# Kernel tuning notes

Measured on AMD Instinct MI355X. Metric: run time of the kernel, lower is better.

## Reference

```python
import jax, jax.numpy as jnp
import numpy as np

INPUT, OUTPUT, HIDDEN, EMBED = 20000, 2048, 1024, 512
BATCH, NUM_GENES = 512, 20000

def _linear_init(key, fan_in, fan_out):
    kw, kb = jax.random.split(key)
    bound = 1.0 / np.sqrt(fan_in)
    W = jax.random.uniform(kw, (fan_out, fan_in), minval=-bound, maxval=bound, dtype=jnp.float32)
    b = jax.random.uniform(kb, (fan_out,), minval=-bound, maxval=bound, dtype=jnp.float32)
    return W, b

def setup_inputs() -> dict:
    key = jax.random.key(0)
    kx, ke, k1, k2, k3 = jax.random.split(key, 5)
    x = jax.random.normal(kx, (BATCH, INPUT), dtype=jnp.float32)
    embedding_x = jax.random.normal(ke, (NUM_GENES, EMBED), dtype=jnp.float32)
    W_ge, b_ge = _linear_init(k1, INPUT, HIDDEN)   # gene_expander Linear
    W_em, b_em = _linear_init(k2, EMBED, HIDDEN)   # embed_mlp Linear
    W_c, b_c = _linear_init(k3, 2 * HIDDEN, OUTPUT)  # combiner Linear
    return {"x": x, "embedding_x": embedding_x, "W_ge": W_ge, "b_ge": b_ge,
            "W_em": W_em, "b_em": b_em, "W_c": W_c, "b_c": b_c}

def reference(x, embedding_x, W_ge, b_ge, W_em, b_em, W_c, b_c):
    lrelu = lambda v: jax.nn.leaky_relu(v, negative_slope=0.01)
    # gene_expander: [B, input] -> [B, hidden]
    x_expanded = lrelu(x @ W_ge.T + b_ge)
    # embed_mlp (dropout = identity at eval): [G, embed] -> [G, hidden]
    gene_embeddings = lrelu(embedding_x @ W_em.T + b_em)
    # softmax over features, then batched GEMM replaces the per-sample loop
    num_genes = min(x.shape[1], gene_embeddings.shape[0])
    weights = jax.nn.softmax(x, axis=1)
    weighted_embeddings = weights[:, :num_genes] @ gene_embeddings[:num_genes]  # [B, hidden]
    combined = jnp.concatenate([x_expanded, weighted_embeddings], axis=1)  # [B, 2*hidden]
    return lrelu(combined @ W_c.T + b_c)  # [B, output]
```

## Files before the change

kernel.cpp:

```cpp
#include <hip/hip_runtime.h>
#include <hip/hip_bf16.h>
#include <stdint.h>

#define BATCH  512
#define INPUT  20000
#define KPAD   20032
#define NPADE  20096
#define HIDDEN 1024
#define EMBED  512
#define NOUT   2048

typedef __attribute__((ext_vector_type(8))) __bf16 bf16x8;
typedef __attribute__((ext_vector_type(8))) unsigned short u16x8;
typedef __attribute__((ext_vector_type(4))) unsigned short u16x4;
typedef __attribute__((ext_vector_type(4))) float f32x4;

static __device__ __forceinline__ unsigned short f2bf(float f) {
  uint32_t u = __builtin_bit_cast(uint32_t, f);
  u += 0x7fffu + ((u >> 16) & 1u);
  return (unsigned short)(u >> 16);
}

static __device__ __forceinline__ void g2l16(const unsigned short* g, unsigned short* l) {
  __builtin_amdgcn_global_load_lds(
      (const __attribute__((address_space(1))) void*)g,
      (__attribute__((address_space(3))) void*)l, 16, 0, 0);
}

__global__ __launch_bounds__(256) void convert_kernel(
    const float* __restrict__ src, unsigned short* __restrict__ dst,
    int rows, int cols, int rowsPad, int colsPad)
{
  const int cpc = colsPad >> 3;
  const int nchunks = rowsPad * cpc;
  for (int idx = blockIdx.x * 256 + threadIdx.x; idx < nchunks; idx += gridDim.x * 256) {
    int row = idx / cpc;
    int c0  = (idx - row * cpc) << 3;
    u16x8 v = {};
    if (row < rows && c0 < cols) {
      const float* p = src + (size_t)row * cols + c0;
      f32x4 f0 = *reinterpret_cast<const f32x4*>(p);
      f32x4 f1 = *reinterpret_cast<const f32x4*>(p + 4);
      v[0] = f2bf(f0[0]); v[1] = f2bf(f0[1]); v[2] = f2bf(f0[2]); v[3] = f2bf(f0[3]);
      v[4] = f2bf(f1[0]); v[5] = f2bf(f1[1]); v[6] = f2bf(f1[2]); v[7] = f2bf(f1[3]);
    }
    *reinterpret_cast<u16x8*>(dst + (size_t)row * colsPad + c0) = v;
  }
}

template<int EPI, int FUSED, int ZBITS>
__global__ __launch_bounds__(256) void gemm97(
    const unsigned short* __restrict__ A0, const unsigned short* __restrict__ B0,
    const unsigned short* __restrict__ A1, const unsigned short* __restrict__ B1,
    int lda, int ldb,
    const float* __restrict__ bias,
    void* __restrict__ Cp, int ldc, int pstride,
    int M, int N, int Nw, int K, int kChunk)
{
  __shared__ __align__(16) unsigned short As[128 * 64];
  __shared__ __align__(16) unsigned short Bs[128 * 64];

  const int zall  = blockIdx.z;
  const int which = FUSED ? (zall >> ZBITS) : 0;
  const int z     = FUSED ? (zall & ((1 << ZBITS) - 1)) : zall;
  const unsigned short* A = (FUSED && which) ? A1 : A0;
  const unsigned short* B = (FUSED && which) ? B1 : B0;

  const int m0 = blockIdx.y * 128, n0 = blockIdx.x * 128;
  const int k0   = z * kChunk;
  const int kend = min(K, k0 + kChunk);
  const int tid = threadIdx.x;
  const int l = tid & 63, w = tid >> 6;

  const int srow = w * 32 + (l >> 3);
  const int scol = (l & 7) * 8;
  const unsigned short* ag = A + (size_t)(m0 + srow) * lda + scol;
  const unsigned short* bg = B + (size_t)(n0 + srow) * ldb + scol;

  const int wm = (w >> 1) * 64, wn = (w & 1) * 64;
  const int lr = l & 15, lk = (l >> 4) * 8;

  f32x4 acc[4][4] = {};

  for (int kb = k0; kb < kend; kb += 64) {
#pragma unroll
    for (int j = 0; j < 4; ++j)
      g2l16(ag + (size_t)j * 8 * lda + kb, As + (w * 32 + j * 8) * 64);
#pragma unroll
    for (int j = 0; j < 4; ++j)
      g2l16(bg + (size_t)j * 8 * ldb + kb, Bs + (w * 32 + j * 8) * 64);
    __syncthreads();
#pragma unroll
    for (int ks = 0; ks < 2; ++ks) {
      bf16x8 a[4], b[4];
#pragma unroll
      for (int i = 0; i < 4; ++i)
        a[i] = *reinterpret_cast<const bf16x8*>(&As[(wm + i * 16 + lr) * 64 + ks * 32 + lk]);
#pragma unroll
      for (int i = 0; i < 4; ++i)
        b[i] = *reinterpret_cast<const bf16x8*>(&Bs[(wn + i * 16 + lr) * 64 + ks * 32 + lk]);
#pragma unroll
      for (int mi = 0; mi < 4; ++mi)
#pragma unroll
        for (int ni = 0; ni < 4; ++ni)
          acc[mi][ni] = __builtin_amdgcn_mfma_f32_16x16x32_bf16(a[mi], b[ni], acc[mi][ni], 0, 0, 0);
    }
    __syncthreads();
  }

  const int rb = (l >> 4) * 4;
#pragma unroll
  for (int mi = 0; mi < 4; ++mi) {
#pragma unroll
    for (int ni = 0; ni < 4; ++ni) {
#pragma unroll
      for (int j = 0; j < 4; ++j) {
        int m = m0 + wm + mi * 16 + rb + j;
        int n = n0 + wn + ni * 16 + lr;
        float v = acc[mi][ni][j];
        if (EPI == 0) {
          if (n < Nw) {
            float t = v + bias[m];
            t = t > 0.f ? t : 0.01f * t;
            reinterpret_cast<unsigned short*>(Cp)[(size_t)m * ldc + n] =
                (n < N) ? f2bf(t) : (unsigned short)0;
          }
        } else {
          reinterpret_cast<float*>(Cp)[(size_t)z * pstride + (size_t)m * ldc +
                                       (FUSED ? which * 1024 : 0) + n] = v;
        }
      }
    }
  }
}

__global__ __launch_bounds__(256) void prep_x_kernel(
    const float* __restrict__ x,
    unsigned short* __restrict__ xb,
    unsigned short* __restrict__ wb)
{
  const int r = blockIdx.x;
  const int t = threadIdx.x;
  const float* xr = x + (size_t)r * INPUT;

  float m = -3.4e38f, s = 0.f;
  for (int c = t; c < INPUT / 4; c += 256) {
    float4 v = reinterpret_cast<const float4*>(xr)[c];
    float cm = fmaxf(fmaxf(v.x, v.y), fmaxf(v.z, v.w));
    if (cm > m) { s *= __expf(m - cm); m = cm; }
    s += __expf(v.x - m) + __expf(v.y - m) + __expf(v.z - m) + __expf(v.w - m);
  }
#pragma unroll
  for (int off = 32; off > 0; off >>= 1) {
    float om = __shfl_xor(m, off);
    float os = __shfl_xor(s, off);
    float nm = fmaxf(m, om);
    s = s * __expf(m - nm) + os * __expf(om - nm);
    m = nm;
  }
  __shared__ float sm[4], ss[4];
  if ((t & 63) == 0) { sm[t >> 6] = m; ss[t >> 6] = s; }
  __syncthreads();
  float M4 = fmaxf(fmaxf(sm[0], sm[1]), fmaxf(sm[2], sm[3]));
  float S4 = ss[0] * __expf(sm[0] - M4) + ss[1] * __expf(sm[1] - M4)
           + ss[2] * __expf(sm[2] - M4) + ss[3] * __expf(sm[3] - M4);
  float inv = 1.f / S4;

  unsigned short* xbr = xb + (size_t)r * KPAD;
  unsigned short* wbr = wb + (size_t)r * KPAD;
  for (int c = t; c < KPAD / 4; c += 256) {
    u16x4 xo = {}, wo = {};
    if (c < INPUT / 4) {
      float4 v = reinterpret_cast<const float4*>(xr)[c];
      xo[0] = f2bf(v.x); xo[1] = f2bf(v.y); xo[2] = f2bf(v.z); xo[3] = f2bf(v.w);
      wo[0] = f2bf(__expf(v.x - M4) * inv);
      wo[1] = f2bf(__expf(v.y - M4) * inv);
      wo[2] = f2bf(__expf(v.z - M4) * inv);
      wo[3] = f2bf(__expf(v.w - M4) * inv);
    }
    reinterpret_cast<u16x4*>(xbr)[c] = xo;
    reinterpret_cast<u16x4*>(wbr)[c] = wo;
  }
}

template<int S, int MODE>
__global__ __launch_bounds__(256) void reduce_kernel(
    const float* __restrict__ P, const float* __restrict__ bias, void* __restrict__ outp)
{
  size_t base = ((size_t)blockIdx.x * 256 + threadIdx.x) * 4;
  f32x4 s = {};
#pragma unroll
  for (int zz = 0; zz < S; ++zz)
    s += *reinterpret_cast<const f32x4*>(P + (size_t)zz * BATCH * NOUT + base);
  int n = (int)(base & (NOUT - 1));
  if (MODE == 0) {
    u16x4 o;
    if (n < 1024) {
#pragma unroll
      for (int j = 0; j < 4; ++j) {
        float v = s[j] + bias[n + j];
        v = v > 0.f ? v : 0.01f * v;
        o[j] = f2bf(v);
      }
    } else {
#pragma unroll
      for (int j = 0; j < 4; ++j) o[j] = f2bf(s[j]);
    }
    *reinterpret_cast<u16x4*>(reinterpret_cast<unsigned short*>(outp) + base) = o;
  } else {
    f32x4 o;
#pragma unroll
    for (int j = 0; j < 4; ++j) {
      float v = s[j] + bias[n + j];
      o[j] = v > 0.f ? v : 0.01f * v;
    }
    *reinterpret_cast<f32x4*>(reinterpret_cast<float*>(outp) + base) = o;
  }
}

extern "C" void kernel_launch(void* const* d_in, const int* in_sizes, int n_in,
                              void* d_out, int out_size, void* d_ws, size_t ws_size,
                              hipStream_t stream)
{
  const float* x    = (const float*)d_in[0];
  const float* emb  = (const float*)d_in[1];
  const float* W_ge = (const float*)d_in[2];
  const float* b_ge = (const float*)d_in[3];
  const float* W_em = (const float*)d_in[4];
  const float* b_em = (const float*)d_in[5];
  const float* W_c  = (const float*)d_in[6];
  const float* b_c  = (const float*)d_in[7];
  float* out = (float*)d_out;

  char* ws = (char*)d_ws;
  unsigned short* xb   = (unsigned short*)(ws);
  unsigned short* wb   = (unsigned short*)(ws + 20512768);
  unsigned short* Wgeb = (unsigned short*)(ws + 41025536);
  unsigned short* Et   = (unsigned short*)(ws + 82051072);
  unsigned short* Wcb  = (unsigned short*)(ws + 123076608);
  unsigned short* comb = (unsigned short*)(ws + 131465216);
  float*          P    = (float*)(ws + 133562368);
  unsigned short* embb = (unsigned short*)(ws + 133562368);
  unsigned short* Wemb = (unsigned short*)(ws + 133562368 + 20578304);

  convert_kernel<<<1024, 256, 0, stream>>>(emb,  embb, INPUT, EMBED, NPADE, EMBED);
  convert_kernel<<<256,  256, 0, stream>>>(W_em, Wemb, HIDDEN, EMBED, HIDDEN, EMBED);
  convert_kernel<<<1024, 256, 0, stream>>>(W_ge, Wgeb, HIDDEN, INPUT, HIDDEN, KPAD);
  convert_kernel<<<512,  256, 0, stream>>>(W_c,  Wcb,  NOUT, NOUT, NOUT, NOUT);

  prep_x_kernel<<<BATCH, 256, 0, stream>>>(x, xb, wb);

  gemm97<0, 0, 0><<<dim3(157, 8, 1), 256, 0, stream>>>(
      Wemb, embb, nullptr, nullptr, EMBED, EMBED, b_em,
      Et, KPAD, 0, HIDDEN, INPUT, KPAD, EMBED, EMBED);

  gemm97<1, 1, 4><<<dim3(8, 4, 32), 256, 0, stream>>>(
      xb, Wgeb, wb, Et, KPAD, KPAD, nullptr,
      P, NOUT, BATCH * NOUT, BATCH, 1024, 1024, KPAD, 1280);

  reduce_kernel<16, 0><<<(BATCH * NOUT / 4) / 256, 256, 0, stream>>>(P, b_ge, comb);

  gemm97<1, 0, 0><<<dim3(16, 4, 4), 256, 0, stream>>>(
      comb, Wcb, nullptr, nullptr, NOUT, NOUT, nullptr,
      P, NOUT, BATCH * NOUT, BATCH, NOUT, NOUT, NOUT, 512);

  reduce_kernel<4, 1><<<(BATCH * NOUT / 4) / 256, 256, 0, stream>>>(P, b_c, out);
}
```

Measured before the change: 256.4 us.

## Add double-buffered 256x256-tile MFMA GEMM for embed and fused K-split GEMMs

Introduces a new GEMM kernel with 256x256 output tiles, 512 threads (8 waves, each computing a 128x64 sub-tile), and double-buffered LDS staging via global_load_lds, so the next K-slice prefetch overlaps MFMA work. It replaces the 128x128 kernel for the embedding MLP GEMM and the fused gene-expander/weighted-embedding split-K GEMM, cutting redundant global/L2 reads of A and B panels. NPADE is raised so the gene dimension pads to a multiple of 256, and the workspace offset is shifted to match. The trade-off is 128 KB of LDS per block and large accumulator register use, which allows only one block per CU and a coarser grid with fewer blocks to hide latency.

```diff
diff --git a/kernel.cpp b/kernel.cpp
--- a/kernel.cpp
+++ b/kernel.cpp
@@ -5,7 +5,7 @@
 #define BATCH  512
 #define INPUT  20000
 #define KPAD   20032
-#define NPADE  20096
+#define NPADE  20224
 #define HIDDEN 1024
 #define EMBED  512
 #define NOUT   2048
@@ -45,6 +45,109 @@
       v[4] = f2bf(f1[0]); v[5] = f2bf(f1[1]); v[6] = f2bf(f1[2]); v[7] = f2bf(f1[3]);
     }
     *reinterpret_cast<u16x8*>(dst + (size_t)row * colsPad + c0) = v;
+  }
+}
+
+template<int EPI, int FUSED, int ZBITS>
+__global__ __launch_bounds__(512, 2) void gemm256(
+    const unsigned short* __restrict__ A0, const unsigned short* __restrict__ B0,
+    const unsigned short* __restrict__ A1, const unsigned short* __restrict__ B1,
+    int lda, int ldb,
+    const float* __restrict__ bias,
+    void* __restrict__ Cp, int ldc, int pstride,
+    int M, int N, int Nw, int K, int kChunk)
+{
+  __shared__ __align__(16) unsigned short As[2][256 * 64];
+  __shared__ __align__(16) unsigned short Bs[2][256 * 64];
+
+  const int zall  = blockIdx.z;
+  const int which = FUSED ? (zall >> ZBITS) : 0;
+  const int z     = FUSED ? (zall & ((1 << ZBITS) - 1)) : zall;
+  const unsigned short* A = (FUSED && which) ? A1 : A0;
+  const unsigned short* B = (FUSED && which) ? B1 : B0;
+
+  const int m0 = blockIdx.y * 256, n0 = blockIdx.x * 256;
+  const int k0   = z * kChunk;
+  const int kend = min(K, k0 + kChunk);
+  const int nt   = (kend - k0) >> 6;
+
+  const int tid = threadIdx.x;
+  const int l = tid & 63, w = tid >> 6;
+
+  const int srow = tid >> 3;
+  const int scol = (tid & 7) * 8;
+  const unsigned short* ag = A + (size_t)(m0 + srow) * lda + scol;
+  const unsigned short* bg = B + (size_t)(n0 + srow) * ldb + scol;
+
+  const int wr = w >> 2, wc = w & 3;
+  const int lr = l & 15, lk = (l >> 4) * 8;
+
+  f32x4 acc[8][4] = {};
+
+#define STAGE(buf, kb)                                                        \
+  do {                                                                        \
+    _Pragma("unroll")                                                         \
+    for (int r = 0; r < 4; ++r)                                               \
+      g2l16(ag + (size_t)(r * 64) * lda + (kb), &As[buf][(r * 64 + w * 8) * 64]); \
+    _Pragma("unroll")                                                         \
+    for (int r = 0; r < 4; ++r)                                               \
+      g2l16(bg + (size_t)(r * 64) * ldb + (kb), &Bs[buf][(r * 64 + w * 8) * 64]); \
+  } while (0)
+
+  STAGE(0, k0);
+  __syncthreads();
+
+  int cur = 0;
+  for (int t = 0; t < nt; ++t) {
+    if (t + 1 < nt) {
+      if (cur) STAGE(0, k0 + (t + 1) * 64);
+      else     STAGE(1, k0 + (t + 1) * 64);
+    }
+#pragma unroll
+    for (int ks = 0; ks < 2; ++ks) {
+      bf16x8 a[8], b[4];
+#pragma unroll
+      for (int i = 0; i < 8; ++i)
+        a[i] = *reinterpret_cast<const bf16x8*>(
+            &As[cur][(wr * 128 + i * 16 + lr) * 64 + ks * 32 + lk]);
+#pragma unroll
+      for (int i = 0; i < 4; ++i)
+        b[i] = *reinterpret_cast<const bf16x8*>(
+            &Bs[cur][(wc * 64 + i * 16 + lr) * 64 + ks * 32 + lk]);
+#pragma unroll
+      for (int mi = 0; mi < 8; ++mi)
+#pragma unroll
+        for (int ni = 0; ni < 4; ++ni)
+          acc[mi][ni] = __builtin_amdgcn_mfma_f32_16x16x32_bf16(a[mi], b[ni], acc[mi][ni], 0, 0, 0);
+    }
+    __syncthreads();
+    cur ^= 1;
+  }
+#undef STAGE
+
+  const int rb = (l >> 4) * 4;
+#pragma unroll
+  for (int mi = 0; mi < 8; ++mi) {
+#pragma unroll
+    for (int ni = 0; ni < 4; ++ni) {
+#pragma unroll
+      for (int j = 0; j < 4; ++j) {
+        int m = m0 + wr * 128 + mi * 16 + rb + j;
+        int n = n0 + wc * 64 + ni * 16 + lr;
+        float v = acc[mi][ni][j];
+        if (EPI == 0) {
+          if (n < Nw) {
+            float t2 = v + bias[m];
+            t2 = t2 > 0.f ? t2 : 0.01f * t2;
+            reinterpret_cast<unsigned short*>(Cp)[(size_t)m * ldc + n] =
+                (n < N) ? f2bf(t2) : (unsigned short)0;
+          }
+        } else {
+          reinterpret_cast<float*>(Cp)[(size_t)z * pstride + (size_t)m * ldc +
+                                       (FUSED ? which * 1024 : 0) + n] = v;
+        }
+      }
+    }
   }
 }
 
@@ -241,7 +344,7 @@
   unsigned short* comb = (unsigned short*)(ws + 131465216);
   float*          P    = (float*)(ws + 133562368);
   unsigned short* embb = (unsigned short*)(ws + 133562368);
-  unsigned short* Wemb = (unsigned short*)(ws + 133562368 + 20578304);
+  unsigned short* Wemb = (unsigned short*)(ws + 133562368 + 20709376);
 
   convert_kernel<<<1024, 256, 0, stream>>>(emb,  embb, INPUT, EMBED, NPADE, EMBED);
   convert_kernel<<<256,  256, 0, stream>>>(W_em, Wemb, HIDDEN, EMBED, HIDDEN, EMBED);
@@ -250,11 +353,11 @@
 
   prep_x_kernel<<<BATCH, 256, 0, stream>>>(x, xb, wb);
 
-  gemm97<0, 0, 0><<<dim3(157, 8, 1), 256, 0, stream>>>(
+  gemm256<0, 0, 0><<<dim3(79, 4, 1), 512, 0, stream>>>(
       Wemb, embb, nullptr, nullptr, EMBED, EMBED, b_em,
       Et, KPAD, 0, HIDDEN, INPUT, KPAD, EMBED, EMBED);
 
-  gemm97<1, 1, 4><<<dim3(8, 4, 32), 256, 0, stream>>>(
+  gemm256<1, 1, 4><<<dim3(4, 2, 32), 512, 0, stream>>>(
       xb, Wgeb, wb, Et, KPAD, KPAD, nullptr,
       P, NOUT, BATCH * NOUT, BATCH, 1024, 1024, KPAD, 1280);
 
```

Result: faster. 248.2 us (-3.2%).

## Replace big split-K GEMM with 256x256 double-buffered, 8-wave pipelined kernel

Applied to the files above, without the earlier changes.

The main fused split-K GEMM (x·W_ge and softmax·embeddings) moves from a 128x128, 4-wave, single-buffered kernel to a 256x256 tile with 8 waves and double-buffered LDS. Global-to-LDS loads for later K tiles are interleaved with four MFMA phases, using explicit waitcnt, barriers and s_setprio. The goal is to hide load latency and raise MFMA reuse per byte loaded. The cost is 128KB of LDS per block and far fewer blocks (256 vs 1024), which risks lower occupancy and load imbalance across CUs.

```diff
diff --git a/kernel.cpp b/kernel.cpp
--- a/kernel.cpp
+++ b/kernel.cpp
@@ -25,6 +25,238 @@
   __builtin_amdgcn_global_load_lds(
       (const __attribute__((address_space(1))) void*)g,
       (__attribute__((address_space(3))) void*)l, 16, 0, 0);
+}
+
+#define MFMA(a, b, c) __builtin_amdgcn_mfma_f32_16x16x32_bf16((a), (b), (c), 0, 0, 0)
+
+__global__ __launch_bounds__(512, 2) void gemm8p_fused(
+    const unsigned short* __restrict__ xb, const unsigned short* __restrict__ Wgeb,
+    const unsigned short* __restrict__ wb, const unsigned short* __restrict__ Etp,
+    float* __restrict__ P, int kChunk)
+{
+  __shared__ __align__(16) unsigned short As[2][2][128 * 64];
+  __shared__ __align__(16) unsigned short Bs[2][2][128 * 64];
+  unsigned short* AsW = &As[0][0][0];
+  unsigned short* BsW = &Bs[0][0][0];
+
+  const int which = blockIdx.z >> 4;
+  const int z     = blockIdx.z & 15;
+  const unsigned short* Ap = which ? wb  : xb;
+  const unsigned short* Bp = which ? Etp : Wgeb;
+
+  const int m0 = blockIdx.y * 256, n0 = blockIdx.x * 256;
+  const int k0   = z * kChunk;
+  const int kend = min(KPAD, k0 + kChunk);
+  const int nt   = (kend - k0) >> 6;
+
+  const int tid = threadIdx.x;
+  const int l = tid & 63, w = tid >> 6;
+  const int srow = tid >> 3, scol = (tid & 7) * 8;
+
+  const unsigned short* ag = Ap + (size_t)(m0 + srow) * KPAD + k0 + scol;
+  const unsigned short* bg = Bp + (size_t)(n0 + srow) * KPAD + k0 + scol;
+
+  const int wr = w >> 2, wc = w & 3;
+  const int lr = l & 15, lk = (l >> 4) * 8;
+
+  auto stA = [&](int buf, int h, int dk) {
+    const unsigned short* g = ag + (size_t)(h * 128) * KPAD + dk;
+    unsigned short* d = AsW + (buf * 2 + h) * 8192 + (w * 8) * 64;
+    g2l16(g, d);
+    g2l16(g + (size_t)64 * KPAD, d + 64 * 64);
+  };
+  auto stB = [&](int buf, int h, int dk) {
+    const unsigned short* g = bg + (size_t)(h * 128) * KPAD + dk;
+    unsigned short* d = BsW + (buf * 2 + h) * 8192 + (w * 8) * 64;
+    g2l16(g, d);
+    g2l16(g + (size_t)64 * KPAD, d + 64 * 64);
+  };
+  auto rdA = [&](int buf, int mi, int ks) -> bf16x8 {
+    return *reinterpret_cast<const bf16x8*>(
+        AsW + (buf * 2 + wr) * 8192 + (mi * 16 + lr) * 64 + ks * 32 + lk);
+  };
+  auto rdB = [&](int buf, int ni, int ks) -> bf16x8 {
+    return *reinterpret_cast<const bf16x8*>(
+        BsW + (buf * 2 + (wc >> 1)) * 8192 + ((wc & 1) * 64 + ni * 16 + lr) * 64 + ks * 32 + lk);
+  };
+
+  f32x4 acc[8][4] = {};
+
+  stA(0, 0, 0); stB(0, 0, 0); stA(0, 1, 0); stB(0, 1, 0);
+  if (nt > 1) {
+    stA(1, 0, 64); stB(1, 0, 64);
+    asm volatile("s_waitcnt vmcnt(4)" ::: "memory");
+  } else {
+    asm volatile("s_waitcnt vmcnt(0)" ::: "memory");
+  }
+  __builtin_amdgcn_s_barrier();
+
+  for (int t = 0; t < nt; ++t) {
+    const int buf = t & 1, nb = buf ^ 1;
+    const int dk1 = (t + 1) << 6, dk2 = (t + 2) << 6;
+    bf16x8 a0[4][2], a1[4][2], b0[2][2], b1[2][2];
+
+#pragma unroll
+    for (int mi = 0; mi < 4; ++mi) { a0[mi][0] = rdA(buf, mi, 0); a0[mi][1] = rdA(buf, mi, 1); }
+#pragma unroll
+    for (int ni = 0; ni < 2; ++ni) { b0[ni][0] = rdB(buf, ni, 0); b0[ni][1] = rdB(buf, ni, 1); }
+    if (t + 1 < nt) stA(nb, 1, dk1);
+    __builtin_amdgcn_s_barrier();
+    asm volatile("s_waitcnt lgkmcnt(0)" ::: "memory");
+    __builtin_amdgcn_sched_barrier(0);
+    __builtin_amdgcn_s_setprio(1);
+#pragma unroll
+    for (int mi = 0; mi < 4; ++mi)
+#pragma unroll
+      for (int ni = 0; ni < 2; ++ni) {
+        acc[mi][ni] = MFMA(a0[mi][0], b0[ni][0], acc[mi][ni]);
+        acc[mi][ni] = MFMA(a0[mi][1], b0[ni][1], acc[mi][ni]);
+      }
+    __builtin_amdgcn_s_setprio(0);
+    __builtin_amdgcn_s_barrier();
+
+#pragma unroll
+    for (int mi = 0; mi < 4; ++mi) { a1[mi][0] = rdA(buf, mi + 4, 0); a1[mi][1] = rdA(buf, mi + 4, 1); }
+    if (t + 1 < nt) stB(nb, 1, dk1);
+    __builtin_amdgcn_s_barrier();
+    asm volatile("s_waitcnt lgkmcnt(0)" ::: "memory");
+    __builtin_amdgcn_sched_barrier(0);
+    __builtin_amdgcn_s_setprio(1);
+#pragma unroll
+    for (int mi = 0; mi < 4; ++mi)
+#pragma unroll
+      for (int ni = 0; ni < 2; ++ni) {
+        acc[mi + 4][ni] = MFMA(a1[mi][0], b0[ni][0], acc[mi + 4][ni]);
+        acc[mi + 4][ni] = MFMA(a1[mi][1], b0[ni][1], acc[mi + 4][ni]);
+      }
+    __builtin_amdgcn_s_setprio(0);
+    __builtin_amdgcn_s_barrier();
+
+#pragma unroll
+    for (int ni = 0; ni < 2; ++ni) { b1[ni][0] = rdB(buf, ni + 2, 0); b1[ni][1] = rdB(buf, ni + 2, 1); }
+    if (t + 2 < nt) stA(buf, 0, dk2);
+    __builtin_amdgcn_s_barrier();
+    asm volatile("s_waitcnt lgkmcnt(0)" ::: "memory");
+    __builtin_amdgcn_sched_barrier(0);
+    __builtin_amdgcn_s_setprio(1);
+#pragma unroll
+    for (int mi = 0; mi < 4; ++mi)
+#pragma unroll
+      for (int ni = 0; ni < 2; ++ni) {
+        acc[mi + 4][ni + 2] = MFMA(a1[mi][0], b1[ni][0], acc[mi + 4][ni + 2]);
+        acc[mi + 4][ni + 2] = MFMA(a1[mi][1], b1[ni][1], acc[mi + 4][ni + 2]);
+      }
+    __builtin_amdgcn_s_setprio(0);
+    __builtin_amdgcn_s_barrier();
+
+    if (t + 2 < nt) stB(buf, 0, dk2);
+    __builtin_amdgcn_s_barrier();
+    __builtin_amdgcn_sched_barrier(0);
+    __builtin_amdgcn_s_setprio(1);
+#pragma unroll
+    for (int mi = 0; mi < 4; ++mi)
+#pragma unroll
+      for (int ni = 0; ni < 2; ++ni) {
+        acc[mi][ni + 2] = MFMA(a0[mi][0], b1[ni][0], acc[mi][ni + 2]);
+        acc[mi][ni + 2] = MFMA(a0[mi][1], b1[ni][1], acc[mi][ni + 2]);
+      }
+    __builtin_amdgcn_s_setprio(0);
+    if (t + 2 < nt)      asm volatile("s_waitcnt vmcnt(4)" ::: "memory");
+    else if (t + 1 < nt) asm volatile("s_waitcnt vmcnt(0)" ::: "memory");
+    __builtin_amdgcn_s_barrier();
+  }
+
+  const int rb = (l >> 4) * 4;
+  float* dst = P + (size_t)z * (BATCH * NOUT) + which * 1024;
+#pragma unroll
+  for (int mi = 0; mi < 8; ++mi)
+#pragma unroll
+    for (int ni = 0; ni < 4; ++ni)
+#pragma unroll
+      for (int j = 0; j < 4; ++j) {
+        int m = m0 + wr * 128 + mi * 16 + rb + j;
+        int n = n0 + wc * 64 + ni * 16 + lr;
+        dst[(size_t)m * NOUT + n] = acc[mi][ni][j];
+      }
+}
+
+template<int EPI>
+__global__ __launch_bounds__(256) void gemm97(
+    const unsigned short* __restrict__ A, const unsigned short* __restrict__ B,
+    int lda, int ldb,
+    const float* __restrict__ bias,
+    void* __restrict__ Cp, int ldc, int pstride,
+    int M, int N, int Nw, int K, int kChunk)
+{
+  __shared__ __align__(16) unsigned short As[128 * 64];
+  __shared__ __align__(16) unsigned short Bs[128 * 64];
+
+  const int z = blockIdx.z;
+  const int m0 = blockIdx.y * 128, n0 = blockIdx.x * 128;
+  const int k0   = z * kChunk;
+  const int kend = min(K, k0 + kChunk);
+  const int tid = threadIdx.x;
+  const int l = tid & 63, w = tid >> 6;
+
+  const int srow = w * 32 + (l >> 3);
+  const int scol = (l & 7) * 8;
+  const unsigned short* ag = A + (size_t)(m0 + srow) * lda + scol;
+  const unsigned short* bg = B + (size_t)(n0 + srow) * ldb + scol;
+
+  const int wm = (w >> 1) * 64, wn = (w & 1) * 64;
+  const int lr = l & 15, lk = (l >> 4) * 8;
+
+  f32x4 acc[4][4] = {};
+
+  for (int kb = k0; kb < kend; kb += 64) {
+#pragma unroll
+    for (int j = 0; j < 4; ++j)
+      g2l16(ag + (size_t)j * 8 * lda + kb, As + (w * 32 + j * 8) * 64);
+#pragma unroll
+    for (int j = 0; j < 4; ++j)
+      g2l16(bg + (size_t)j * 8 * ldb + kb, Bs + (w * 32 + j * 8) * 64);
+    __syncthreads();
+#pragma unroll
+    for (int ks = 0; ks < 2; ++ks) {
+      bf16x8 a[4], b[4];
+#pragma unroll
+      for (int i = 0; i < 4; ++i)
+        a[i] = *reinterpret_cast<const bf16x8*>(&As[(wm + i * 16 + lr) * 64 + ks * 32 + lk]);
+#pragma unroll
+      for (int i = 0; i < 4; ++i)
+        b[i] = *reinterpret_cast<const bf16x8*>(&Bs[(wn + i * 16 + lr) * 64 + ks * 32 + lk]);
+#pragma unroll
+      for (int mi = 0; mi < 4; ++mi)
+#pragma unroll
+        for (int ni = 0; ni < 4; ++ni)
+          acc[mi][ni] = MFMA(a[mi], b[ni], acc[mi][ni]);
+    }
+    __syncthreads();
+  }
+
+  const int rb = (l >> 4) * 4;
+#pragma unroll
+  for (int mi = 0; mi < 4; ++mi) {
+#pragma unroll
+    for (int ni = 0; ni < 4; ++ni) {
+#pragma unroll
+      for (int j = 0; j < 4; ++j) {
+        int m = m0 + wm + mi * 16 + rb + j;
+        int n = n0 + wn + ni * 16 + lr;
+        float v = acc[mi][ni][j];
+        if (EPI == 0) {
+          if (n < Nw) {
+            float t = v + bias[m];
+            t = t > 0.f ? t : 0.01f * t;
+            reinterpret_cast<unsigned short*>(Cp)[(size_t)m * ldc + n] =
+                (n < N) ? f2bf(t) : (unsigned short)0;
+          }
+        } else {
+          reinterpret_cast<float*>(Cp)[(size_t)z * pstride + (size_t)m * ldc + n] = v;
+        }
+      }
+    }
+  }
 }
 
 __global__ __launch_bounds__(256) void convert_kernel(
@@ -48,92 +280,6 @@
   }
 }
 
-template<int EPI, int FUSED, int ZBITS>
-__global__ __launch_bounds__(256) void gemm97(
-    const unsigned short* __restrict__ A0, const unsigned short* __restrict__ B0,
-    const unsigned short* __restrict__ A1, const unsigned short* __restrict__ B1,
-    int lda, int ldb,
-    const float* __restrict__ bias,
-    void* __restrict__ Cp, int ldc, int pstride,
-    int M, int N, int Nw, int K, int kChunk)
-{
-  __shared__ __align__(16) unsigned short As[128 * 64];
-  __shared__ __align__(16) unsigned short Bs[128 * 64];
-
-  const int zall  = blockIdx.z;
-  const int which = FUSED ? (zall >> ZBITS) : 0;
-  const int z     = FUSED ? (zall & ((1 << ZBITS) - 1)) : zall;
-  const unsigned short* A = (FUSED && which) ? A1 : A0;
-  const unsigned short* B = (FUSED && which) ? B1 : B0;
-
-  const int m0 = blockIdx.y * 128, n0 = blockIdx.x * 128;
-  const int k0   = z * kChunk;
-  const int kend = min(K, k0 + kChunk);
-  const int tid = threadIdx.x;
-  const int l = tid & 63, w = tid >> 6;
-
-  const int srow = w * 32 + (l >> 3);
-  const int scol = (l & 7) * 8;
-  const unsigned short* ag = A + (size_t)(m0 + srow) * lda + scol;
-  const unsigned short* bg = B + (size_t)(n0 + srow) * ldb + scol;
-
-  const int wm = (w >> 1) * 64, wn = (w & 1) * 64;
-  const int lr = l & 15, lk = (l >> 4) * 8;
-
-  f32x4 acc[4][4] = {};
-
-  for (int kb = k0; kb < kend; kb += 64) {
-#pragma unroll
-    for (int j = 0; j < 4; ++j)
-      g2l16(ag + (size_t)j * 8 * lda + kb, As + (w * 32 + j * 8) * 64);
-#pragma unroll
-    for (int j = 0; j < 4; ++j)
-      g2l16(bg + (size_t)j * 8 * ldb + kb, Bs + (w * 32 + j * 8) * 64);
-    __syncthreads();
-#pragma unroll
-    for (int ks = 0; ks < 2; ++ks) {
-      bf16x8 a[4], b[4];
-#pragma unroll
-      for (int i = 0; i < 4; ++i)
-        a[i] = *reinterpret_cast<const bf16x8*>(&As[(wm + i * 16 + lr) * 64 + ks * 32 + lk]);
-#pragma unroll
-      for (int i = 0; i < 4; ++i)
-        b[i] = *reinterpret_cast<const bf16x8*>(&Bs[(wn + i * 16 + lr) * 64 + ks * 32 + lk]);
-#pragma unroll
-      for (int mi = 0; mi < 4; ++mi)
-#pragma unroll
-        for (int ni = 0; ni < 4; ++ni)
-          acc[mi][ni] = __builtin_amdgcn_mfma_f32_16x16x32_bf16(a[mi], b[ni], acc[mi][ni], 0, 0, 0);
-    }
-    __syncthreads();
-  }
-
-  const int rb = (l >> 4) * 4;
-#pragma unroll
-  for (int mi = 0; mi < 4; ++mi) {
-#pragma unroll
-    for (int ni = 0; ni < 4; ++ni) {
-#pragma unroll
-      for (int j = 0; j < 4; ++j) {
-        int m = m0 + wm + mi * 16 + rb + j;
-        int n = n0 + wn + ni * 16 + lr;
-        float v = acc[mi][ni][j];
-        if (EPI == 0) {
-          if (n < Nw) {
-            float t = v + bias[m];
-            t = t > 0.f ? t : 0.01f * t;
-            reinterpret_cast<unsigned short*>(Cp)[(size_t)m * ldc + n] =
-                (n < N) ? f2bf(t) : (unsigned short)0;
-          }
-        } else {
-          reinterpret_cast<float*>(Cp)[(size_t)z * pstride + (size_t)m * ldc +
-                                       (FUSED ? which * 1024 : 0) + n] = v;
-        }
-      }
-    }
-  }
-}
-
 __global__ __launch_bounds__(256) void prep_x_kernel(
     const float* __restrict__ x,
     unsigned short* __restrict__ xb,
@@ -250,18 +396,16 @@
 
   prep_x_kernel<<<BATCH, 256, 0, stream>>>(x, xb, wb);
 
-  gemm97<0, 0, 0><<<dim3(157, 8, 1), 256, 0, stream>>>(
-      Wemb, embb, nullptr, nullptr, EMBED, EMBED, b_em,
+  gemm97<0><<<dim3(157, 8, 1), 256, 0, stream>>>(
+      Wemb, embb, EMBED, EMBED, b_em,
       Et, KPAD, 0, HIDDEN, INPUT, KPAD, EMBED, EMBED);
 
-  gemm97<1, 1, 4><<<dim3(8, 4, 32), 256, 0, stream>>>(
-      xb, Wgeb, wb, Et, KPAD, KPAD, nullptr,
-      P, NOUT, BATCH * NOUT, BATCH, 1024, 1024, KPAD, 1280);
+  gemm8p_fused<<<dim3(4, 2, 32), 512, 0, stream>>>(xb, Wgeb, wb, Et, P, 1280);
 
   reduce_kernel<16, 0><<<(BATCH * NOUT / 4) / 256, 256, 0, stream>>>(P, b_ge, comb);
 
-  gemm97<1, 0, 0><<<dim3(16, 4, 4), 256, 0, stream>>>(
-      comb, Wcb, nullptr, nullptr, NOUT, NOUT, nullptr,
+  gemm97<1><<<dim3(16, 4, 4), 256, 0, stream>>>(
+      comb, Wcb, NOUT, NOUT, nullptr,
       P, NOUT, BATCH * NOUT, BATCH, NOUT, NOUT, NOUT, 512);
 
   reduce_kernel<4, 1><<<(BATCH * NOUT / 4) / 256, 256, 0, stream>>>(P, b_c, out);
```

Measured after the change: 242.6 us. -5.4%, faster.
